# Kernel optimization log

Hardware: AMD Instinct MI355X
Metric: run time of the kernel (lower is better)

## Reference

```python
import jax, jax.numpy as jnp
import numpy as np

N = 2048
IN_CH = 64
HID = 16
OUT_CH = 8
NUM_GRAPHS = 64


def setup_inputs() -> dict:
    key = jax.random.key(0)
    ks = jax.random.split(key, 12)
    x_batch = jax.random.normal(ks[0], (N, IN_CH), dtype=jnp.float32)
    # BFS distances in [0, 10], -1 marks cross-graph pairs
    dist_batch = (jax.random.randint(ks[1], (N, N), 0, 12) - 1).astype(jnp.float32)
    batch_vector = jnp.sort(jax.random.randint(ks[2], (N,), 0, NUM_GRAPHS)).astype(jnp.int32)
    s1 = 1.0  # Linear(1, HID) fan_in = 1
    s2 = 1.0 / np.sqrt(HID)
    # per-feature scalar MLPs, stacked over the feature axis
    fs_w1 = jax.random.uniform(ks[3], (IN_CH, HID), minval=-s1, maxval=s1, dtype=jnp.float32)
    fs_b1 = jax.random.uniform(ks[4], (IN_CH, HID), minval=-s1, maxval=s1, dtype=jnp.float32)
    fs_w2 = jax.random.uniform(ks[5], (IN_CH, HID, OUT_CH), minval=-s2, maxval=s2, dtype=jnp.float32)
    fs_b2 = jax.random.uniform(ks[6], (IN_CH, OUT_CH), minval=-s2, maxval=s2, dtype=jnp.float32)
    # rho MLP on scalar distances
    rho_w1 = jax.random.uniform(ks[7], (HID,), minval=-s1, maxval=s1, dtype=jnp.float32)
    rho_b1 = jax.random.uniform(ks[8], (HID,), minval=-s1, maxval=s1, dtype=jnp.float32)
    rho_w2 = jax.random.uniform(ks[9], (HID, OUT_CH), minval=-s2, maxval=s2, dtype=jnp.float32)
    rho_b2 = jax.random.uniform(ks[10], (OUT_CH,), minval=-s2, maxval=s2, dtype=jnp.float32)
    return dict(x_batch=x_batch, dist_batch=dist_batch, batch_vector=batch_vector,
                fs_w1=fs_w1, fs_b1=fs_b1, fs_w2=fs_w2, fs_b2=fs_b2,
                rho_w1=rho_w1, rho_b1=rho_b1, rho_w2=rho_w2, rho_b2=rho_b2)


def reference(x_batch, dist_batch, batch_vector,
              fs_w1, fs_b1, fs_w2, fs_b2,
              rho_w1, rho_b1, rho_w2, rho_b2):
    # Per-feature scalar MLPs: fx[n,f,c] = fs_f(x[n,f])  -> [N, F, C]
    h = jax.nn.relu(x_batch[:, :, None] * fs_w1[None] + fs_b1[None])       # [N,F,H]
    fx = jnp.einsum('nfh,fhc->nfc', h, fs_w2) + fs_b2[None]                # [N,F,C]
    # matmul over NxN then sum over features == contract with fx summed over f
    g = fx.sum(axis=1)                                                     # [N,C]
    # rho applied elementwise to each distance scalar
    dh = jax.nn.relu(dist_batch[:, :, None] * rho_w1 + rho_b1)             # [N,N,H]
    dist_embed = jnp.einsum('nmh,hc->nmc', dh, rho_w2) + rho_b2            # [N,N,C]
    dist_embed = jnp.where((dist_batch >= 0)[:, :, None], dist_embed, 0.0)
    mf = jnp.einsum('nmc,mc->nc', dist_embed, g)                           # [N,C]
    # graph pooling via scatter-add
    out = jax.ops.segment_sum(mf, batch_vector, num_segments=NUM_GRAPHS)   # [G,C]
    return out
```

## Files before the change

kernel.cpp:

```cpp
#include <hip/hip_runtime.h>
#include <hip/hip_fp16.h>

#define NN 2048
#define FF 64
#define HH 16
#define CC 8

template <int CTRL>
__device__ __forceinline__ float dpp_step(float x) {
  return x + __int_as_float(
      __builtin_amdgcn_update_dpp(0, __float_as_int(x), CTRL, 0xf, 0xf, false));
}
__device__ __forceinline__ float wave64_sum(float x) {
  x = dpp_step<0x111>(x);
  x = dpp_step<0x112>(x);
  x = dpp_step<0x114>(x);
  x = dpp_step<0x118>(x);
  x = dpp_step<0x142>(x);
  x = dpp_step<0x143>(x);
  return x;
}

__global__ __launch_bounds__(256, 1) void k1_g_lut(
    const float* __restrict__ x, const float* __restrict__ fw1,
    const float* __restrict__ fb1, const float* __restrict__ fw2,
    const float* __restrict__ fb2, const float* __restrict__ rw1,
    const float* __restrict__ rb1, const float* __restrict__ rw2,
    const float* __restrict__ rb2, __half* __restrict__ gout,
    __half* __restrict__ lutout, float* __restrict__ out) {
  const int tid = threadIdx.x;
  if (blockIdx.x == 256) {
    if (tid < 128) {
      const int v = tid >> 3, c = tid & 7;
      float acc = 0.f;
      if (v <= 10) {
        acc = rb2[c];
#pragma unroll
        for (int h = 0; h < HH; ++h) {
          const float hv = fmaxf(fmaf((float)v, rw1[h], rb1[h]), 0.f);
          acc = fmaf(hv, rw2[h * CC + c], acc);
        }
      }
      lutout[v * CC + c] = __float2half(acc);
    } else {
      ((float4*)out)[tid - 128] = make_float4(0.f, 0.f, 0.f, 0.f);
    }
    return;
  }
  const int grp = tid >> 7;
  const int t = tid & 127;
  const int h = t >> 3, c = t & 7;
  const int group = blockIdx.x * 2 + grp;
  float w1r[FF], b1r[FF], w2r[FF];
#pragma unroll
  for (int f = 0; f < FF; ++f) {
    w1r[f] = fw1[f * HH + h];
    b1r[f] = fb1[f * HH + h];
    w2r[f] = fw2[f * (HH * CC) + t];
  }
  float s2 = 0.f;
#pragma unroll
  for (int f = 0; f < FF; ++f) s2 += fb2[f * CC + c];
  __shared__ float red[2][8];
  for (int i = 0; i < 4; ++i) {
    const int n = group * 4 + i;
    const float* xr = x + n * FF;
    float acc = 0.f;
#pragma unroll
    for (int f = 0; f < FF; ++f) {
      const float hv = fmaxf(fmaf(xr[f], w1r[f], b1r[f]), 0.f);
      acc = fmaf(hv, w2r[f], acc);
    }
    acc += __shfl_xor(acc, 8);
    acc += __shfl_xor(acc, 16);
    acc += __shfl_xor(acc, 32);
    if (t >= 64 && t < 72) red[grp][t - 64] = acc;
    __syncthreads();
    if (t < 8) gout[n * CC + t] = __float2half(acc + red[grp][t] + s2);
    __syncthreads();
  }
}

__global__ __launch_bounds__(256, 2) void k3_main(
    const float* __restrict__ dist, const int* __restrict__ batch,
    const __half* __restrict__ gws, const __half* __restrict__ lutws,
    const float* __restrict__ rw1, const float* __restrict__ rb1,
    const float* __restrict__ rw2, const float* __restrict__ rb2,
    float* __restrict__ out) {
  __shared__ uint4 gl[NN];
  __shared__ uint4 lutl[16];
  const int tid = threadIdx.x;
#pragma unroll
  for (int k = 0; k < 8; ++k) {
    const int row = k * 256 + tid;
    gl[row ^ ((row >> 3) & 7)] = ((const uint4*)gws)[row];
  }
  if (tid < 16) lutl[tid] = ((const uint4*)lutws)[tid];
  __syncthreads();

  const int wave = tid >> 6, lane = tid & 63;
  const int n = blockIdx.x * 4 + wave;
  const float4* row4 = (const float4*)(dist + (size_t)n * NN);
  const int s3 = (lane >> 1) & 3;
  const int s4 = (lane >> 1) & 4;
  float acc[8] = {0.f, 0.f, 0.f, 0.f, 0.f, 0.f, 0.f, 0.f};
#pragma unroll
  for (int it = 0; it < 8; ++it) {
    const float4 d4 = row4[it * 64 + lane];
    const int vb = (it * 256 + 4 * lane) ^ s4;
#pragma unroll
    for (int j = 0; j < 4; ++j) {
      const float d = (&d4.x)[j];
      const int di = (int)d;
      const bool lutok = ((float)di == d) && (d >= 0.f) && (di <= 10);
      const int idx = lutok ? di : 15;
      const uint4 gv = gl[vb + (j ^ s3)];
      const uint4 lv = lutl[idx];
      const __half2* gh = (const __half2*)&gv;
      const __half2* lh = (const __half2*)&lv;
#pragma unroll
      for (int q = 0; q < 4; ++q) {
        const float2 gf = __half22float2(gh[q]);
        const float2 lf = __half22float2(lh[q]);
        acc[2 * q] = fmaf(gf.x, lf.x, acc[2 * q]);
        acc[2 * q + 1] = fmaf(gf.y, lf.y, acc[2 * q + 1]);
      }
      if (__builtin_expect((d >= 0.f) && !lutok, 0)) {
        float e[8];
#pragma unroll
        for (int cc = 0; cc < 8; ++cc) e[cc] = rb2[cc];
#pragma unroll
        for (int hh = 0; hh < 16; ++hh) {
          const float hv = fmaxf(fmaf(d, rw1[hh], rb1[hh]), 0.f);
#pragma unroll
          for (int cc = 0; cc < 8; ++cc) e[cc] = fmaf(hv, rw2[hh * 8 + cc], e[cc]);
        }
        const __half* gh8 = (const __half*)&gv;
#pragma unroll
        for (int cc = 0; cc < 8; ++cc)
          acc[cc] = fmaf(e[cc], __half2float(gh8[cc]), acc[cc]);
      }
    }
  }
  float tot[8];
#pragma unroll
  for (int cc = 0; cc < 8; ++cc) tot[cc] = wave64_sum(acc[cc]);
  if (lane == 63) {
    const int gb = batch[n] * CC;
#pragma unroll
    for (int cc = 0; cc < 8; ++cc) atomicAdd(&out[gb + cc], tot[cc]);
  }
}

extern "C" void kernel_launch(void* const* d_in, const int* in_sizes, int n_in,
                              void* d_out, int out_size, void* d_ws,
                              size_t ws_size, hipStream_t stream) {
  const float* x = (const float*)d_in[0];
  const float* dist = (const float*)d_in[1];
  const int* batch = (const int*)d_in[2];
  const float* fw1 = (const float*)d_in[3];
  const float* fb1 = (const float*)d_in[4];
  const float* fw2 = (const float*)d_in[5];
  const float* fb2 = (const float*)d_in[6];
  const float* rw1 = (const float*)d_in[7];
  const float* rb1 = (const float*)d_in[8];
  const float* rw2 = (const float*)d_in[9];
  const float* rb2 = (const float*)d_in[10];
  float* out = (float*)d_out;
  __half* gws = (__half*)d_ws;
  __half* lutws = (__half*)((char*)d_ws + 32768);
  k1_g_lut<<<257, 256, 0, stream>>>(x, fw1, fb1, fw2, fb2, rw1, rb1, rw2, rb2,
                                    gws, lutws, out);
  k3_main<<<512, 256, 0, stream>>>(dist, batch, gws, lutws, rw1, rb1, rw2, rb2,
                                   out);
}
```

Before: 109.7 us.

## Split each distance row across two waves, read g from global, accumulate in half2

The main kernel stops staging the full 32KB g table in shared memory and instead reads g vectors straight from global/L2 per chunk. Each row is now split between two waves, so twice as many blocks are launched with a higher occupancy bound. Per-chunk partial sums use packed half-precision FMA before converting to fp32, which cuts conversion and FMA instruction count but lowers accumulation precision. The LUT validity check drops the d>=0 test: -1 distances map to the zero LUT slot through the index mask.

```diff
diff --git a/kernel.cpp b/kernel.cpp
--- a/kernel.cpp
+++ b/kernel.cpp
@@ -81,51 +81,46 @@
   }
 }
 
-__global__ __launch_bounds__(256, 2) void k3_main(
+__global__ __launch_bounds__(256, 4) void k3_main(
     const float* __restrict__ dist, const int* __restrict__ batch,
     const __half* __restrict__ gws, const __half* __restrict__ lutws,
     const float* __restrict__ rw1, const float* __restrict__ rb1,
     const float* __restrict__ rw2, const float* __restrict__ rb2,
     float* __restrict__ out) {
-  __shared__ uint4 gl[NN];
   __shared__ uint4 lutl[16];
   const int tid = threadIdx.x;
-#pragma unroll
-  for (int k = 0; k < 8; ++k) {
-    const int row = k * 256 + tid;
-    gl[row ^ ((row >> 3) & 7)] = ((const uint4*)gws)[row];
-  }
   if (tid < 16) lutl[tid] = ((const uint4*)lutws)[tid];
   __syncthreads();
 
   const int wave = tid >> 6, lane = tid & 63;
-  const int n = blockIdx.x * 4 + wave;
+  const int W = blockIdx.x * 4 + wave;
+  const int n = W >> 1, half = W & 1;
   const float4* row4 = (const float4*)(dist + (size_t)n * NN);
-  const int s3 = (lane >> 1) & 3;
-  const int s4 = (lane >> 1) & 4;
+  const uint4* gp = (const uint4*)gws;
   float acc[8] = {0.f, 0.f, 0.f, 0.f, 0.f, 0.f, 0.f, 0.f};
 #pragma unroll
-  for (int it = 0; it < 8; ++it) {
-    const float4 d4 = row4[it * 64 + lane];
-    const int vb = (it * 256 + 4 * lane) ^ s4;
+  for (int it = 0; it < 4; ++it) {
+    const int chunk = half * 4 + it;
+    const float4 d4 = row4[chunk * 64 + lane];
+    const int mbase = chunk * 256 + 4 * lane;
+    uint4 gv[4];
+#pragma unroll
+    for (int j = 0; j < 4; ++j) gv[j] = gp[mbase + j];
+    __half2 acch[4];
+#pragma unroll
+    for (int q = 0; q < 4; ++q) acch[q] = __float2half2_rn(0.f);
 #pragma unroll
     for (int j = 0; j < 4; ++j) {
       const float d = (&d4.x)[j];
       const int di = (int)d;
-      const bool lutok = ((float)di == d) && (d >= 0.f) && (di <= 10);
-      const int idx = lutok ? di : 15;
-      const uint4 gv = gl[vb + (j ^ s3)];
+      const bool ok = ((float)di == d) && (di <= 10);
+      const int idx = ok ? (di & 15) : 15;
       const uint4 lv = lutl[idx];
-      const __half2* gh = (const __half2*)&gv;
+      const __half2* gh = (const __half2*)&gv[j];
       const __half2* lh = (const __half2*)&lv;
 #pragma unroll
-      for (int q = 0; q < 4; ++q) {
-        const float2 gf = __half22float2(gh[q]);
-        const float2 lf = __half22float2(lh[q]);
-        acc[2 * q] = fmaf(gf.x, lf.x, acc[2 * q]);
-        acc[2 * q + 1] = fmaf(gf.y, lf.y, acc[2 * q + 1]);
-      }
-      if (__builtin_expect((d >= 0.f) && !lutok, 0)) {
+      for (int q = 0; q < 4; ++q) acch[q] = __hfma2(gh[q], lh[q], acch[q]);
+      if (__builtin_expect((d >= 0.f) && !ok, 0)) {
         float e[8];
 #pragma unroll
         for (int cc = 0; cc < 8; ++cc) e[cc] = rb2[cc];
@@ -135,11 +130,17 @@
 #pragma unroll
           for (int cc = 0; cc < 8; ++cc) e[cc] = fmaf(hv, rw2[hh * 8 + cc], e[cc]);
         }
-        const __half* gh8 = (const __half*)&gv;
+        const __half* gh8 = (const __half*)&gv[j];
 #pragma unroll
         for (int cc = 0; cc < 8; ++cc)
           acc[cc] = fmaf(e[cc], __half2float(gh8[cc]), acc[cc]);
       }
+    }
+#pragma unroll
+    for (int q = 0; q < 4; ++q) {
+      const float2 f2 = __half22float2(acch[q]);
+      acc[2 * q] += f2.x;
+      acc[2 * q + 1] += f2.y;
     }
   }
   float tot[8];
@@ -171,6 +172,6 @@
   __half* lutws = (__half*)((char*)d_ws + 32768);
   k1_g_lut<<<257, 256, 0, stream>>>(x, fw1, fb1, fw2, fb2, rw1, rb1, rw2, rb2,
                                     gws, lutws, out);
-  k3_main<<<512, 256, 0, stream>>>(dist, batch, gws, lutws, rw1, rb1, rw2, rb2,
-                                   out);
+  k3_main<<<1024, 256, 0, stream>>>(dist, batch, gws, lutws, rw1, rb1, rw2, rb2,
+                                    out);
 }
```

New measurement: 128.3 us. 1.17x slower.
